# Kernel optimization log

Measured on AMD Instinct MI355X. Metric: run time of the kernel, lower is better.

## Reference

```python
import jax, jax.numpy as jnp
import numpy as np

K = 16  # kNN size (self included)
R = 4   # upsampling ratio


def _knn(pts, k):
    # pts: (B,N,3) -> idx (B,N,k); smallest distance first, so idx[:,:,0] is self
    sq = jnp.sum(pts * pts, axis=-1)
    d = sq[:, :, None] - 2.0 * jnp.einsum('bnd,bmd->bnm', pts, pts) + sq[:, None, :]
    _, idx = jax.lax.top_k(-d, k)
    return idx


def _gather(feats, idx):
    # feats (B,N,C), idx (B,N,k) -> (B,N,k,C)
    return jax.vmap(lambda f, i: f[i])(feats, idx)


def _conv1d(x, w, b):  # pointwise Conv1d: x (B,C,N)
    return jnp.einsum('oc,bcn->bon', w, x) + b[None, :, None]


def _conv2d(x, w, b):  # pointwise Conv2d: x (B,C,N,K)
    return jnp.einsum('oc,bcnk->bonk', w, x) + b[None, :, None, None]


def setup_inputs() -> dict:
    key = jax.random.key(0)
    ks = jax.random.split(key, 16)
    B, N = 2, 8192
    w = lambda k, s: jax.random.normal(k, s, jnp.float32) * 0.1
    return {
        'x': jax.random.normal(ks[0], (B, 3, N), jnp.float32),
        'mlp1_w1': w(ks[1], (32, 3)), 'mlp1_b1': jnp.zeros((32,), jnp.float32),
        'mlp1_w2': w(ks[2], (64, 32)), 'mlp1_b2': jnp.zeros((64,), jnp.float32),
        'mlp2_w1': w(ks[3], (32, 9)), 'mlp2_b1': jnp.zeros((32,), jnp.float32),
        'mlp3_w1': w(ks[4], (128, 96)), 'mlp3_b1': jnp.zeros((128,), jnp.float32),
        'mlp3_w2': w(ks[5], (12, 128)), 'mlp3_b2': jnp.zeros((12,), jnp.float32),
        'att_w1': w(ks[6], (128, 64)), 'att_b1': jnp.zeros((128,), jnp.float32),
        'att_w2': w(ks[7], (64, 128)), 'att_b2': jnp.zeros((64,), jnp.float32),
    }


def reference(x, mlp1_w1, mlp1_b1, mlp1_w2, mlp1_b2, mlp2_w1, mlp2_b1,
              mlp3_w1, mlp3_b1, mlp3_w2, mlp3_b2,
              att_w1, att_b1, att_w2, att_b2):
    B, C, N = x.shape
    pts = jnp.transpose(x, (0, 2, 1))                     # (B,N,3)
    idx = _knn(jax.lax.stop_gradient(pts), K)             # (B,N,K)

    # local 3x3 covariance features -> (B,9,N)
    nb = _gather(pts, idx)                                # (B,N,K,3)
    c = nb - jnp.mean(nb, axis=2, keepdims=True)
    cov = jnp.einsum('bnki,bnkj->bnij', c, c) / K         # (B,N,3,3)
    cov_feat = jnp.transpose(cov.reshape(B, N, 9), (0, 2, 1))

    # mlp1: 3 -> 32 -> 64, relu on both (last_act=True)
    f1 = jax.nn.relu(_conv1d(jax.nn.relu(_conv1d(x, mlp1_w1, mlp1_b1)), mlp1_w2, mlp1_b2))

    # gather neighbor features (exclude self) and form relative features
    fk = _gather(jnp.transpose(f1, (0, 2, 1)), idx[:, :, 1:])   # (B,N,K-1,64)
    f_knn = jnp.transpose(fk, (0, 3, 1, 2)) - f1[:, :, :, None]  # (B,64,N,K-1)

    # attention MLP (2D): 64 -> 128 -> 64, softmax over neighbor axis
    h = jax.nn.relu(_conv2d(f_knn, att_w1, att_b1))
    w = jax.nn.softmax(_conv2d(h, att_w2, att_b2), axis=-1)
    f_agg = jnp.sum(w * f_knn, axis=-1)                   # (B,64,N)

    # mlp2: 9 -> 32 with relu
    f_cov = jax.nn.relu(_conv1d(cov_feat, mlp2_w1, mlp2_b1))     # (B,32,N)

    f = jnp.concatenate([f_agg, f_cov], axis=1)           # (B,96,N)
    g = _conv1d(jax.nn.relu(_conv1d(f, mlp3_w1, mlp3_b1)), mlp3_w2, mlp3_b2)  # (B,3R,N)

    return jnp.tile(x, (1, 1, R)) + 0.15 * g.reshape(B, -1, R * N)
```

## Files before the change

### kernel.cpp

```cpp
#include <hip/hip_runtime.h>

#define BB 2
#define NN 8192
#define KK 16
#define QPB 64
#define PRE 256
#define CAP 16
typedef unsigned long long ull;
typedef unsigned short ushort;
#define KINF 0xFFFFFFFFFFFFFFFFULL

typedef __attribute__((ext_vector_type(8))) short short8;
typedef __attribute__((ext_vector_type(4))) float f32x4;

static __device__ __forceinline__ ushort f2bf(float f) {
    unsigned u = __float_as_uint(f);
    unsigned r = (u + 0x7FFFu + ((u >> 16) & 1u)) >> 16;
    return (ushort)r;
}
static __device__ __forceinline__ float bf2f(ushort s) {
    return __uint_as_float(((unsigned)s) << 16);
}

static __device__ __forceinline__ float distq(const float4& qp, const float4& cn) {
    return fmaf(qp.x, cn.x, fmaf(qp.y, cn.y, fmaf(qp.z, cn.z, __fadd_rn(qp.w, cn.w))));
}

__global__ __launch_bounds__(256) void prep_f1_kernel(
    const float* __restrict__ x, float4* __restrict__ pts4, float4* __restrict__ pts4n,
    const float* __restrict__ w1, const float* __restrict__ b1,
    const float* __restrict__ w2, const float* __restrict__ b2,
    ushort* __restrict__ f1)
{
    if (blockIdx.x < 64) {
        int t = blockIdx.x * 256 + threadIdx.x;
        int b = t >> 13, n = t & (NN - 1);
        float x0 = x[(b * 3 + 0) * NN + n];
        float x1 = x[(b * 3 + 1) * NN + n];
        float x2 = x[(b * 3 + 2) * NN + n];
        float sq = fmaf(x2, x2, fmaf(x1, x1, __fmul_rn(x0, x0)));
        pts4[t]  = make_float4(x0, x1, x2, sq);
        pts4n[t] = make_float4(-2.f * x0, -2.f * x1, -2.f * x2, sq);
    } else {
        int P = (blockIdx.x - 64) * 256 + threadIdx.x;
        int b = P >> 13, n = P & (NN - 1);
        float x0 = x[(b * 3 + 0) * NN + n];
        float x1 = x[(b * 3 + 1) * NN + n];
        float x2 = x[(b * 3 + 2) * NN + n];
        float h[32];
#pragma unroll
        for (int o = 0; o < 32; ++o) {
            float v = fmaf(w1[o * 3 + 2], x2, fmaf(w1[o * 3 + 1], x1, fmaf(w1[o * 3 + 0], x0, b1[o])));
            h[o] = fmaxf(v, 0.f);
        }
#pragma unroll
        for (int o4 = 0; o4 < 16; ++o4) {
            float vv[4];
#pragma unroll
            for (int u = 0; u < 4; ++u) {
                int o = o4 * 4 + u;
                float v = b2[o];
#pragma unroll
                for (int k = 0; k < 32; ++k) v = fmaf(w2[o * 32 + k], h[k], v);
                vv[u] = fmaxf(v, 0.f);
            }
            ushort4 s = { f2bf(vv[0]), f2bf(vv[1]), f2bf(vv[2]), f2bf(vv[3]) };
            *(ushort4*)(f1 + (size_t)P * 64 + o4 * 4) = s;
        }
    }
}

__global__ __launch_bounds__(512) void knn_prefix_kernel(
    const float4* __restrict__ pts4, const float4* __restrict__ pts4n,
    float* __restrict__ thrb)
{
    __shared__ float pbuf[11 * 512];
    __shared__ float smem[8 * 4 * 64];

    const int t    = threadIdx.x;
    const int wv   = t >> 6;
    const int lane = t & 63;
    const int b    = blockIdx.y;
    const int q    = blockIdx.x * QPB + lane;
    const int sl   = __builtin_amdgcn_readfirstlane(wv);

    const float4 qp = pts4[b * NN + q];
    const float4* __restrict__ cp = pts4n + (size_t)b * NN + (size_t)sl * 1024;

    float l0 = 3.0e38f, l1 = 3.0e38f, l2 = 3.0e38f, l3 = 3.0e38f;
    float curmax = 3.0e38f;
    int pend = 0;

    for (int i0 = 0; i0 < PRE; i0 += 8) {
#pragma unroll
        for (int u = 0; u < 8; ++u) {
            float d = distq(qp, cp[i0 + u]);
            pbuf[pend * 512 + t] = d;
            pend += (d < curmax) ? 1 : 0;
        }
        if (__any(pend >= 4)) {
            for (int j = 0; j < 11; ++j) {
                if (!__any(j < pend)) break;
                float v = pbuf[j * 512 + t];
                float k = (j < pend) ? v : 3.0e38f;
                bool b3 = k < l3, b2 = k < l2, b1 = k < l1, b0 = k < l0;
                l3 = b3 ? (b2 ? l2 : k) : l3;
                l2 = b2 ? (b1 ? l1 : k) : l2;
                l1 = b1 ? (b0 ? l0 : k) : l1;
                l0 = b0 ? k : l0;
            }
            pend = 0;
            curmax = l3;
        }
    }
    for (int j = 0; j < 11; ++j) {
        if (!__any(j < pend)) break;
        float v = pbuf[j * 512 + t];
        float k = (j < pend) ? v : 3.0e38f;
        bool b3 = k < l3, b2 = k < l2, b1 = k < l1, b0 = k < l0;
        l3 = b3 ? (b2 ? l2 : k) : l3;
        l2 = b2 ? (b1 ? l1 : k) : l2;
        l1 = b1 ? (b0 ? l0 : k) : l1;
        l0 = b0 ? k : l0;
    }

    __syncthreads();
    smem[(wv * 4 + 0) * 64 + lane] = l0;
    smem[(wv * 4 + 1) * 64 + lane] = l1;
    smem[(wv * 4 + 2) * 64 + lane] = l2;
    smem[(wv * 4 + 3) * 64 + lane] = l3;
    __syncthreads();

    if (t < QPB) {
        float h[8];
        int kc[8];
#pragma unroll
        for (int s = 0; s < 8; ++s) { h[s] = smem[(s * 4) * 64 + t]; kc[s] = 0; }
        float best = 3.0e38f;
        for (int o = 0; o < KK; ++o) {
            best = h[0]; int bs = 0;
#pragma unroll
            for (int s = 1; s < 8; ++s) { if (h[s] < best) { best = h[s]; bs = s; } }
#pragma unroll
            for (int s = 0; s < 8; ++s) {
                if (s == bs) {
                    kc[s]++;
                    h[s] = (kc[s] < 4) ? smem[(s * 4 + kc[s]) * 64 + t] : 3.0e38f;
                }
            }
        }
        thrb[(size_t)b * NN + blockIdx.x * QPB + t] = best;
    }
}

__global__ __launch_bounds__(512) void knn_scan_kernel(
    const float4* __restrict__ pts4, const float4* __restrict__ pts4n,
    const float* __restrict__ thrb,
    ushort* __restrict__ buf, ushort* __restrict__ cnt)
{
    const int t    = threadIdx.x;
    const int wv   = t >> 6;
    const int lane = t & 63;
    const int b    = blockIdx.y;
    const int q    = blockIdx.x * QPB + lane;
    const int s    = __builtin_amdgcn_readfirstlane(blockIdx.z * 8 + wv);

    const float4 qp = pts4[b * NN + q];
    const float thr = thrb[(size_t)b * NN + q];
    const float4* __restrict__ cp = pts4n + (size_t)b * NN + (size_t)s * 256;
    const unsigned cbase = s * 256;

    const int cell = (((int)(b * NN) + q) << 5) + s;
    ushort* __restrict__ bp = buf + (size_t)cell * CAP;
    int pend = 0;

    for (int i0 = 0; i0 < 256; i0 += 8) {
#pragma unroll
        for (int u = 0; u < 8; ++u) {
            const int ci = i0 + u;
            float d = distq(qp, cp[ci]);
            if (d <= thr) {
                bp[pend & (CAP - 1)] = (ushort)(cbase + ci);
                pend++;
            }
        }
    }
    cnt[cell] = (ushort)((pend < CAP) ? pend : CAP);
}

__global__ __launch_bounds__(256) void knn_select_kernel(
    const float4* __restrict__ pts4, const float4* __restrict__ pts4n,
    const ushort* __restrict__ buf, const ushort* __restrict__ cnt,
    int* __restrict__ iout)
{
    __shared__ ull sm3[4][8][8][KK];

    const int t = threadIdx.x;
    const int wv = t >> 6, lane = t & 63;
    const int qq = lane & 7, hh = lane >> 3;
    const int q  = (blockIdx.x * 4 + wv) * 8 + qq;
    const int b  = q >> 13;

    const float4 qp = pts4[q];
    ull list[KK];
#pragma unroll
    for (int i = 0; i < KK; ++i) list[i] = KINF;

#pragma unroll
    for (int ss = 0; ss < 4; ++ss) {
        const int s = hh * 4 + ss;
        const int cell = (q << 5) + s;
        const int n = cnt[cell];
        const ushort* bp = buf + (size_t)cell * CAP;
        for (int i = 0; i < n; ++i) {
            int id = bp[i];
            float d = distq(qp, pts4n[b * NN + id]);
            unsigned ud = __float_as_uint(d);
            ud ^= ((unsigned)((int)ud >> 31)) | 0x80000000u;
            ull k = ((ull)ud << 32) | (unsigned)id;
#pragma unroll
            for (int i2 = KK - 1; i2 > 0; --i2) {
                bool c1 = k < list[i2];
                bool c2 = k < list[i2 - 1];
                ull nd = c2 ? list[i2 - 1] : k;
                list[i2] = c1 ? nd : list[i2];
            }
            list[0] = (k < list[0]) ? k : list[0];
        }
    }

#pragma unroll
    for (int k = 0; k < KK; ++k) sm3[wv][hh][qq][k] = list[k];

    if (hh == 0) {
        ull h[8]; int kc[8];
#pragma unroll
        for (int s = 0; s < 8; ++s) { h[s] = sm3[wv][s][qq][0]; kc[s] = 0; }
        int* op = iout + (size_t)q * KK;
        for (int o = 0; o < KK; ++o) {
            ull best = h[0]; int bs = 0;
#pragma unroll
            for (int s = 1; s < 8; ++s) { if (h[s] < best) { best = h[s]; bs = s; } }
            op[o] = (int)(unsigned)(best & 0xFFFFFFFFULL);
#pragma unroll
            for (int s = 0; s < 8; ++s) {
                if (s == bs) {
                    kc[s]++;
                    h[s] = (kc[s] < KK) ? sm3[wv][s][qq][kc[s]] : KINF;
                }
            }
        }
    }
}

__global__ __launch_bounds__(256, 2) void attn_cov_kernel(
    const ushort* __restrict__ f1, const int* __restrict__ idx,
    const float* __restrict__ aw1, const float* __restrict__ ab1,
    const float* __restrict__ aw2, const float* __restrict__ ab2,
    ushort* __restrict__ fagg,
    const float4* __restrict__ pts4,
    const float* __restrict__ cw, const float* __restrict__ cb,
    ushort* __restrict__ fcov)
{
    __shared__ __align__(16) ushort w1l[128][72];
    __shared__ __align__(16) ushort w2l[64][136];
    __shared__ __align__(16) ushort fkb[4][16][72];
    __shared__ __align__(16) ushort hb[4][16][136];

    const int t = threadIdx.x;

    if (blockIdx.x >= 512) {
        int P = (blockIdx.x - 512) * 256 + t;
        int b = P >> 13;
        const int4* ip4 = (const int4*)(idx + (size_t)P * KK);
        int ids[KK];
#pragma unroll
        for (int g = 0; g < 4; ++g) {
            int4 v = ip4[g];
            ids[g * 4 + 0] = v.x; ids[g * 4 + 1] = v.y;
            ids[g * 4 + 2] = v.z; ids[g * 4 + 3] = v.w;
        }
        float px[KK], py[KK], pz[KK];
#pragma unroll
        for (int k = 0; k < KK; ++k) {
            float4 c = pts4[b * NN + ids[k]];
            px[k] = c.x; py[k] = c.y; pz[k] = c.z;
        }
        float mx = 0.f, my = 0.f, mz = 0.f;
#pragma unroll
        for (int k = 0; k < KK; ++k) { mx += px[k]; my += py[k]; mz += pz[k]; }
        mx *= (1.f / 16.f); my *= (1.f / 16.f); mz *= (1.f / 16.f);
        float c00 = 0, c01 = 0, c02 = 0, c11 = 0, c12 = 0, c22 = 0;
#pragma unroll
        for (int k = 0; k < KK; ++k) {
            float dx = px[k] - mx, dy = py[k] - my, dz = pz[k] - mz;
            c00 = fmaf(dx, dx, c00); c01 = fmaf(dx, dy, c01); c02 = fmaf(dx, dz, c02);
            c11 = fmaf(dy, dy, c11); c12 = fmaf(dy, dz, c12); c22 = fmaf(dz, dz, c22);
        }
        const float inv = 1.f / 16.f;
        float cf[9] = { c00 * inv, c01 * inv, c02 * inv,
                        c01 * inv, c11 * inv, c12 * inv,
                        c02 * inv, c12 * inv, c22 * inv };
        ushort* outp = fcov + (size_t)P * 32;
#pragma unroll
        for (int o = 0; o < 32; ++o) {
            float v = cb[o];
#pragma unroll
            for (int m = 0; m < 9; ++m) v = fmaf(cw[o * 9 + m], cf[m], v);
            outp[o] = f2bf(fmaxf(v, 0.f));
        }
        return;
    }

    const int wv = t >> 6, lane = t & 63;
    const int l15 = lane & 15, qd = lane >> 4;

    for (int i = t; i < 128 * 64; i += 256) {
        int r = i >> 6, c = i & 63;
        w1l[r][c] = f2bf(aw1[i]);
    }
    for (int i = t; i < 64 * 128; i += 256) {
        int r = i >> 7, c = i & 127;
        w2l[r][c] = f2bf(aw2[i]);
    }
    __syncthreads();

    const int W = blockIdx.x * 4 + wv;
    for (int g = 0; g < 8; ++g) {
        const int P = W * 8 + g;
        const int b = P >> 13;

        float fc = bf2f(f1[(size_t)P * 64 + lane]);
        ushort fn[15];
#pragma unroll
        for (int j = 0; j < 15; ++j) {
            int nb = idx[(size_t)P * KK + 1 + j];
            fn[j] = f1[((size_t)b * NN + nb) * 64 + lane];
        }
#pragma unroll
        for (int j = 0; j < 15; ++j) fkb[wv][j][lane] = f2bf(bf2f(fn[j]) - fc);
        fkb[wv][15][lane] = 0;

        short8 a0 = *(const short8*)&fkb[wv][l15][qd * 8];
        short8 a1 = *(const short8*)&fkb[wv][l15][32 + qd * 8];

#pragma unroll
        for (int tile = 0; tile < 8; ++tile) {
            float bv = ab1[tile * 16 + l15];
            f32x4 acc = { bv, bv, bv, bv };
            short8 b0 = *(const short8*)&w1l[tile * 16 + l15][qd * 8];
            short8 b1f = *(const short8*)&w1l[tile * 16 + l15][32 + qd * 8];
            acc = __builtin_amdgcn_mfma_f32_16x16x32_bf16(a0, b0, acc, 0, 0, 0);
            acc = __builtin_amdgcn_mfma_f32_16x16x32_bf16(a1, b1f, acc, 0, 0, 0);
#pragma unroll
            for (int reg = 0; reg < 4; ++reg)
                hb[wv][qd * 4 + reg][tile * 16 + l15] = f2bf(fmaxf(acc[reg], 0.f));
        }

        short8 a2[4];
#pragma unroll
        for (int ks = 0; ks < 4; ++ks)
            a2[ks] = *(const short8*)&hb[wv][l15][ks * 32 + qd * 8];

        f32x4 L[4];
#pragma unroll
        for (int tile = 0; tile < 4; ++tile) {
            float bv = ab2[tile * 16 + l15];
            f32x4 acc = { bv, bv, bv, bv };
#pragma unroll
            for (int ks = 0; ks < 4; ++ks) {
                short8 bf = *(const short8*)&w2l[tile * 16 + l15][ks * 32 + qd * 8];
                acc = __builtin_amdgcn_mfma_f32_16x16x32_bf16(a2[ks], bf, acc, 0, 0, 0);
            }
            L[tile] = acc;
        }

        float fa[4];
#pragma unroll
        for (int tile = 0; tile < 4; ++tile) {
            float m1 = -3.0e38f;
#pragma unroll
            for (int reg = 0; reg < 4; ++reg)
                if (qd * 4 + reg < 15) m1 = fmaxf(m1, L[tile][reg]);
            m1 = fmaxf(m1, __shfl_xor(m1, 16));
            m1 = fmaxf(m1, __shfl_xor(m1, 32));
            float e[4], ssum = 0.f;
#pragma unroll
            for (int reg = 0; reg < 4; ++reg) {
                bool valid = (qd * 4 + reg < 15);
                e[reg] = valid ? __expf(L[tile][reg] - m1) : 0.f;
                ssum += e[reg];
            }
            ssum += __shfl_xor(ssum, 16);
            ssum += __shfl_xor(ssum, 32);
            float part = 0.f;
#pragma unroll
            for (int reg = 0; reg < 4; ++reg) {
                float fkv = bf2f(fkb[wv][qd * 4 + reg][tile * 16 + l15]);
                part = fmaf(e[reg], fkv, part);
            }
            part += __shfl_xor(part, 16);
            part += __shfl_xor(part, 32);
            fa[tile] = part / ssum;
        }
        if (qd == 0) {
#pragma unroll
            for (int tile = 0; tile < 4; ++tile)
                fagg[(size_t)P * 64 + tile * 16 + l15] = f2bf(fa[tile]);
        }
    }
}

__global__ __launch_bounds__(256) void mlp3_kernel(
    const ushort* __restrict__ fagg, const ushort* __restrict__ fcov,
    const float* __restrict__ w1, const float* __restrict__ b1,
    const float* __restrict__ w2, const float* __restrict__ b2,
    const float* __restrict__ x, float* __restrict__ out)
{
    __shared__ __align__(16) ushort fb[4][16][104];
    __shared__ __align__(16) ushort hb[4][16][136];

    const int t = threadIdx.x;
    const int wv = t >> 6, lane = t & 63;
    const int l15 = lane & 15, qd = lane >> 4;

    short8 w1f[8][3];
#pragma unroll
    for (int tile = 0; tile < 8; ++tile)
#pragma unroll
        for (int ks = 0; ks < 3; ++ks) {
            const float* p = w1 + ((size_t)(tile * 16 + l15) * 96 + ks * 32 + qd * 8);
            float4 A = *(const float4*)p, B = *(const float4*)(p + 4);
            short8 f;
            f[0] = f2bf(A.x); f[1] = f2bf(A.y); f[2] = f2bf(A.z); f[3] = f2bf(A.w);
            f[4] = f2bf(B.x); f[5] = f2bf(B.y); f[6] = f2bf(B.z); f[7] = f2bf(B.w);
            w1f[tile][ks] = f;
        }
    short8 w2f[4];
#pragma unroll
    for (int ks = 0; ks < 4; ++ks) {
        short8 f = {};
        if (l15 < 12) {
            const float* p = w2 + ((size_t)l15 * 128 + ks * 32 + qd * 8);
            float4 A = *(const float4*)p, B = *(const float4*)(p + 4);
            f[0] = f2bf(A.x); f[1] = f2bf(A.y); f[2] = f2bf(A.z); f[3] = f2bf(A.w);
            f[4] = f2bf(B.x); f[5] = f2bf(B.y); f[6] = f2bf(B.z); f[7] = f2bf(B.w);
        }
        w2f[ks] = f;
    }

    const int T = blockIdx.x * 4 + wv;

    {
        const int pt = lane >> 2, c4 = lane & 3;
        const ushort* fap = fagg + ((size_t)(T * 16 + pt) * 64 + c4 * 16);
        *(short8*)&fb[wv][pt][c4 * 16]     = *(const short8*)(fap);
        *(short8*)&fb[wv][pt][c4 * 16 + 8] = *(const short8*)(fap + 8);
        const ushort* fcp = fcov + ((size_t)(T * 16 + pt) * 32 + c4 * 8);
        *(short8*)&fb[wv][pt][64 + c4 * 8] = *(const short8*)(fcp);
    }

    short8 a[3];
#pragma unroll
    for (int ks = 0; ks < 3; ++ks)
        a[ks] = *(const short8*)&fb[wv][l15][ks * 32 + qd * 8];

#pragma unroll
    for (int tile = 0; tile < 8; ++tile) {
        float bv = b1[tile * 16 + l15];
        f32x4 acc = { bv, bv, bv, bv };
#pragma unroll
        for (int ks = 0; ks < 3; ++ks)
            acc = __builtin_amdgcn_mfma_f32_16x16x32_bf16(a[ks], w1f[tile][ks], acc, 0, 0, 0);
#pragma unroll
        for (int reg = 0; reg < 4; ++reg)
            hb[wv][qd * 4 + reg][tile * 16 + l15] = f2bf(fmaxf(acc[reg], 0.f));
    }

    short8 a2[4];
#pragma unroll
    for (int ks = 0; ks < 4; ++ks)
        a2[ks] = *(const short8*)&hb[wv][l15][ks * 32 + qd * 8];

    float bv2 = (l15 < 12) ? b2[l15] : 0.f;
    f32x4 acc = { bv2, bv2, bv2, bv2 };
#pragma unroll
    for (int ks = 0; ks < 4; ++ks)
        acc = __builtin_amdgcn_mfma_f32_16x16x32_bf16(a2[ks], w2f[ks], acc, 0, 0, 0);

    if (l15 < 12) {
        const int c = l15 >> 2, rr = l15 & 3;
#pragma unroll
        for (int reg = 0; reg < 4; ++reg) {
            int P = T * 16 + qd * 4 + reg;
            int b = P >> 13, n = P & (NN - 1);
            float xv = x[((size_t)b * 3 + c) * NN + n];
            out[(((size_t)b * 3 + c) * 4 + rr) * NN + n] = xv + 0.15f * acc[reg];
        }
    }
}

extern "C" void kernel_launch(void* const* d_in, const int* in_sizes, int n_in,
                              void* d_out, int out_size, void* d_ws, size_t ws_size,
                              hipStream_t stream)
{
    (void)in_sizes; (void)n_in; (void)out_size; (void)ws_size;
    const float* x    = (const float*)d_in[0];
    const float* m1w1 = (const float*)d_in[1];
    const float* m1b1 = (const float*)d_in[2];
    const float* m1w2 = (const float*)d_in[3];
    const float* m1b2 = (const float*)d_in[4];
    const float* m2w1 = (const float*)d_in[5];
    const float* m2b1 = (const float*)d_in[6];
    const float* m3w1 = (const float*)d_in[7];
    const float* m3b1 = (const float*)d_in[8];
    const float* m3w2 = (const float*)d_in[9];
    const float* m3b2 = (const float*)d_in[10];
    const float* aw1  = (const float*)d_in[11];
    const float* ab1  = (const float*)d_in[12];
    const float* aw2  = (const float*)d_in[13];
    const float* ab2  = (const float*)d_in[14];
    float* out = (float*)d_out;

    char* ws = (char*)d_ws;
    float4* pts4  = (float4*)(ws + 0);
    float4* pts4n = (float4*)(ws + 262144);
    float*  thrb  = (float*)(ws + 524288);
    int*    idxb  = (int*)  (ws + 589824);
    ushort* cntb  = (ushort*)(ws + 1638400);
    ushort* bufb  = (ushort*)(ws + 2686976);
    ushort* f1b   = (ushort*)(ws + 19464192);
    ushort* fagg  = (ushort*)(ws + 21561344);
    ushort* fcov  = (ushort*)(ws + 23658496);

    prep_f1_kernel<<<128, 256, 0, stream>>>(x, pts4, pts4n, m1w1, m1b1, m1w2, m1b2, f1b);
    knn_prefix_kernel<<<dim3(NN / QPB, BB), 512, 0, stream>>>(pts4, pts4n, thrb);
    knn_scan_kernel<<<dim3(NN / QPB, BB, 4), 512, 0, stream>>>(pts4, pts4n, thrb, bufb, cntb);
    knn_select_kernel<<<512, 256, 0, stream>>>(pts4, pts4n, bufb, cntb, idxb);
    attn_cov_kernel<<<576, 256, 0, stream>>>(f1b, idxb, aw1, ab1, aw2, ab2, fagg,
                                             pts4, m2w1, m2b1, fcov);
    mlp3_kernel<<<256, 256, 0, stream>>>(fagg, fcov, m3w1, m3b1, m3w2, m3b2, x, out);
}
```

Measured before the change: 262.8 us.

## Fuse kNN select with attention/cov kernel and ballot-compact the scan

```diff
diff --git a/kernel.cpp b/kernel.cpp
--- a/kernel.cpp
+++ b/kernel.cpp
@@ -162,124 +162,124 @@
     const int wv   = t >> 6;
     const int lane = t & 63;
     const int b    = blockIdx.y;
-    const int q    = blockIdx.x * QPB + lane;
     const int s    = __builtin_amdgcn_readfirstlane(blockIdx.z * 8 + wv);
-
-    const float4 qp = pts4[b * NN + q];
-    const float thr = thrb[(size_t)b * NN + q];
-    const float4* __restrict__ cp = pts4n + (size_t)b * NN + (size_t)s * 256;
+    const int q0   = blockIdx.x * QPB;
     const unsigned cbase = s * 256;
-
-    const int cell = (((int)(b * NN) + q) << 5) + s;
-    ushort* __restrict__ bp = buf + (size_t)cell * CAP;
-    int pend = 0;
-
-    for (int i0 = 0; i0 < 256; i0 += 8) {
-#pragma unroll
-        for (int u = 0; u < 8; ++u) {
-            const int ci = i0 + u;
-            float d = distq(qp, cp[ci]);
-            if (d <= thr) {
-                bp[pend & (CAP - 1)] = (ushort)(cbase + ci);
-                pend++;
-            }
-        }
-    }
-    cnt[cell] = (ushort)((pend < CAP) ? pend : CAP);
-}
-
-__global__ __launch_bounds__(256) void knn_select_kernel(
+    const ull lmask = (lane == 0) ? 0ull : (~0ull >> (64 - lane));
+
+    const float4* __restrict__ cp = pts4n + (size_t)b * NN + cbase;
+    float4 c0 = cp[lane], c1 = cp[64 + lane], c2 = cp[128 + lane], c3 = cp[192 + lane];
+
+    const float4* __restrict__ qpb = pts4 + (size_t)b * NN + q0;
+    const float*  __restrict__ thp = thrb + (size_t)b * NN + q0;
+
+    for (int qi = 0; qi < QPB; ++qi) {
+        const float4 qp = qpb[qi];
+        const float thr = thp[qi];
+        const int cell = (((b * NN) + q0 + qi) << 5) + s;
+        ushort* __restrict__ bp = buf + (size_t)cell * CAP;
+        int pend = 0;
+#pragma unroll
+        for (int k = 0; k < 4; ++k) {
+            float4 c = (k == 0) ? c0 : (k == 1) ? c1 : (k == 2) ? c2 : c3;
+            float d = distq(qp, c);
+            bool pass = (d <= thr);
+            ull m = __ballot(pass);
+            int slot = pend + (int)__popcll(m & lmask);
+            if (pass && slot < CAP) bp[slot] = (ushort)(cbase + k * 64 + lane);
+            pend += (int)__popcll(m);
+        }
+        if (lane == 0) cnt[cell] = (ushort)((pend < CAP) ? pend : CAP);
+    }
+}
+
+__global__ __launch_bounds__(256, 2) void sel_attn_cov_kernel(
     const float4* __restrict__ pts4, const float4* __restrict__ pts4n,
     const ushort* __restrict__ buf, const ushort* __restrict__ cnt,
-    int* __restrict__ iout)
+    const ushort* __restrict__ f1,
+    const float* __restrict__ aw1, const float* __restrict__ ab1,
+    const float* __restrict__ aw2, const float* __restrict__ ab2,
+    const float* __restrict__ cw, const float* __restrict__ cb,
+    ushort* __restrict__ fagg, ushort* __restrict__ fcov)
 {
-    __shared__ ull sm3[4][8][8][KK];
+    __shared__ __align__(16) ull sm3[4][8][8][KK];
+    __shared__ __align__(16) ushort w2l[64][136];
+    __shared__ int idxl[32][KK];
+
+    ushort (*fkb)[16][72]  = (ushort(*)[16][72])sm3;
+    ushort (*hb)[16][136]  = (ushort(*)[16][136])((char*)sm3 + 9216);
 
     const int t = threadIdx.x;
     const int wv = t >> 6, lane = t & 63;
-    const int qq = lane & 7, hh = lane >> 3;
-    const int q  = (blockIdx.x * 4 + wv) * 8 + qq;
-    const int b  = q >> 13;
-
-    const float4 qp = pts4[q];
-    ull list[KK];
-#pragma unroll
-    for (int i = 0; i < KK; ++i) list[i] = KINF;
-
-#pragma unroll
-    for (int ss = 0; ss < 4; ++ss) {
-        const int s = hh * 4 + ss;
-        const int cell = (q << 5) + s;
-        const int n = cnt[cell];
-        const ushort* bp = buf + (size_t)cell * CAP;
-        for (int i = 0; i < n; ++i) {
-            int id = bp[i];
-            float d = distq(qp, pts4n[b * NN + id]);
-            unsigned ud = __float_as_uint(d);
-            ud ^= ((unsigned)((int)ud >> 31)) | 0x80000000u;
-            ull k = ((ull)ud << 32) | (unsigned)id;
-#pragma unroll
-            for (int i2 = KK - 1; i2 > 0; --i2) {
-                bool c1 = k < list[i2];
-                bool c2 = k < list[i2 - 1];
-                ull nd = c2 ? list[i2 - 1] : k;
-                list[i2] = c1 ? nd : list[i2];
-            }
-            list[0] = (k < list[0]) ? k : list[0];
-        }
-    }
-
-#pragma unroll
-    for (int k = 0; k < KK; ++k) sm3[wv][hh][qq][k] = list[k];
-
-    if (hh == 0) {
-        ull h[8]; int kc[8];
-#pragma unroll
-        for (int s = 0; s < 8; ++s) { h[s] = sm3[wv][s][qq][0]; kc[s] = 0; }
-        int* op = iout + (size_t)q * KK;
-        for (int o = 0; o < KK; ++o) {
-            ull best = h[0]; int bs = 0;
-#pragma unroll
-            for (int s = 1; s < 8; ++s) { if (h[s] < best) { best = h[s]; bs = s; } }
-            op[o] = (int)(unsigned)(best & 0xFFFFFFFFULL);
-#pragma unroll
-            for (int s = 0; s < 8; ++s) {
-                if (s == bs) {
-                    kc[s]++;
-                    h[s] = (kc[s] < KK) ? sm3[wv][s][qq][kc[s]] : KINF;
+
+    for (int i = t; i < 64 * 128; i += 256) {
+        int r = i >> 7, c = i & 127;
+        w2l[r][c] = f2bf(aw2[i]);
+    }
+
+    {
+        const int qq = lane & 7, hh = lane >> 3;
+        const int q  = blockIdx.x * 32 + wv * 8 + qq;
+        const int b  = q >> 13;
+
+        const float4 qp = pts4[q];
+        ull list[KK];
+#pragma unroll
+        for (int i = 0; i < KK; ++i) list[i] = KINF;
+
+#pragma unroll
+        for (int ss = 0; ss < 4; ++ss) {
+            const int s = hh * 4 + ss;
+            const int cell = (q << 5) + s;
+            const int n = cnt[cell];
+            const ushort* bp = buf + (size_t)cell * CAP;
+            for (int i = 0; i < n; ++i) {
+                int id = bp[i];
+                float d = distq(qp, pts4n[b * NN + id]);
+                unsigned ud = __float_as_uint(d);
+                ud ^= ((unsigned)((int)ud >> 31)) | 0x80000000u;
+                ull k = ((ull)ud << 32) | (unsigned)id;
+#pragma unroll
+                for (int i2 = KK - 1; i2 > 0; --i2) {
+                    bool c1 = k < list[i2];
+                    bool c2 = k < list[i2 - 1];
+                    ull nd = c2 ? list[i2 - 1] : k;
+                    list[i2] = c1 ? nd : list[i2];
                 }
-            }
-        }
-    }
-}
-
-__global__ __launch_bounds__(256, 2) void attn_cov_kernel(
-    const ushort* __restrict__ f1, const int* __restrict__ idx,
-    const float* __restrict__ aw1, const float* __restrict__ ab1,
-    const float* __restrict__ aw2, const float* __restrict__ ab2,
-    ushort* __restrict__ fagg,
-    const float4* __restrict__ pts4,
-    const float* __restrict__ cw, const float* __restrict__ cb,
-    ushort* __restrict__ fcov)
-{
-    __shared__ __align__(16) ushort w1l[128][72];
-    __shared__ __align__(16) ushort w2l[64][136];
-    __shared__ __align__(16) ushort fkb[4][16][72];
-    __shared__ __align__(16) ushort hb[4][16][136];
-
-    const int t = threadIdx.x;
-
-    if (blockIdx.x >= 512) {
-        int P = (blockIdx.x - 512) * 256 + t;
+                list[0] = (k < list[0]) ? k : list[0];
+            }
+        }
+
+#pragma unroll
+        for (int k = 0; k < KK; ++k) sm3[wv][hh][qq][k] = list[k];
+
+        if (hh == 0) {
+            ull h[8]; int kc[8];
+#pragma unroll
+            for (int s = 0; s < 8; ++s) { h[s] = sm3[wv][s][qq][0]; kc[s] = 0; }
+            for (int o = 0; o < KK; ++o) {
+                ull best = h[0]; int bs = 0;
+#pragma unroll
+                for (int s = 1; s < 8; ++s) { if (h[s] < best) { best = h[s]; bs = s; } }
+                idxl[wv * 8 + qq][o] = (int)(unsigned)(best & 0xFFFFFFFFULL);
+#pragma unroll
+                for (int s = 0; s < 8; ++s) {
+                    if (s == bs) {
+                        kc[s]++;
+                        h[s] = (kc[s] < KK) ? sm3[wv][s][qq][kc[s]] : KINF;
+                    }
+                }
+            }
+        }
+    }
+    __syncthreads();
+
+    if (t < 32) {
+        int P = blockIdx.x * 32 + t;
         int b = P >> 13;
-        const int4* ip4 = (const int4*)(idx + (size_t)P * KK);
         int ids[KK];
 #pragma unroll
-        for (int g = 0; g < 4; ++g) {
-            int4 v = ip4[g];
-            ids[g * 4 + 0] = v.x; ids[g * 4 + 1] = v.y;
-            ids[g * 4 + 2] = v.z; ids[g * 4 + 3] = v.w;
-        }
+        for (int k = 0; k < KK; ++k) ids[k] = idxl[t][k];
         float px[KK], py[KK], pz[KK];
 #pragma unroll
         for (int k = 0; k < KK; ++k) {
@@ -309,32 +309,32 @@
             for (int m = 0; m < 9; ++m) v = fmaf(cw[o * 9 + m], cf[m], v);
             outp[o] = f2bf(fmaxf(v, 0.f));
         }
-        return;
-    }
-
-    const int wv = t >> 6, lane = t & 63;
+    }
+
     const int l15 = lane & 15, qd = lane >> 4;
 
-    for (int i = t; i < 128 * 64; i += 256) {
-        int r = i >> 6, c = i & 63;
-        w1l[r][c] = f2bf(aw1[i]);
-    }
-    for (int i = t; i < 64 * 128; i += 256) {
-        int r = i >> 7, c = i & 127;
-        w2l[r][c] = f2bf(aw2[i]);
-    }
-    __syncthreads();
-
-    const int W = blockIdx.x * 4 + wv;
+    short8 w1f[8][2];
+#pragma unroll
+    for (int tile = 0; tile < 8; ++tile)
+#pragma unroll
+        for (int ks = 0; ks < 2; ++ks) {
+            const float4* p = (const float4*)(aw1 + ((tile * 16 + l15) * 64 + ks * 32 + qd * 8));
+            float4 A = p[0], B = p[1];
+            short8 f;
+            f[0] = f2bf(A.x); f[1] = f2bf(A.y); f[2] = f2bf(A.z); f[3] = f2bf(A.w);
+            f[4] = f2bf(B.x); f[5] = f2bf(B.y); f[6] = f2bf(B.z); f[7] = f2bf(B.w);
+            w1f[tile][ks] = f;
+        }
+
     for (int g = 0; g < 8; ++g) {
-        const int P = W * 8 + g;
+        const int P = blockIdx.x * 32 + wv * 8 + g;
         const int b = P >> 13;
 
         float fc = bf2f(f1[(size_t)P * 64 + lane]);
         ushort fn[15];
 #pragma unroll
         for (int j = 0; j < 15; ++j) {
-            int nb = idx[(size_t)P * KK + 1 + j];
+            int nb = idxl[wv * 8 + g][1 + j];
             fn[j] = f1[((size_t)b * NN + nb) * 64 + lane];
         }
 #pragma unroll
@@ -348,10 +348,8 @@
         for (int tile = 0; tile < 8; ++tile) {
             float bv = ab1[tile * 16 + l15];
             f32x4 acc = { bv, bv, bv, bv };
-            short8 b0 = *(const short8*)&w1l[tile * 16 + l15][qd * 8];
-            short8 b1f = *(const short8*)&w1l[tile * 16 + l15][32 + qd * 8];
-            acc = __builtin_amdgcn_mfma_f32_16x16x32_bf16(a0, b0, acc, 0, 0, 0);
-            acc = __builtin_amdgcn_mfma_f32_16x16x32_bf16(a1, b1f, acc, 0, 0, 0);
+            acc = __builtin_amdgcn_mfma_f32_16x16x32_bf16(a0, w1f[tile][0], acc, 0, 0, 0);
+            acc = __builtin_amdgcn_mfma_f32_16x16x32_bf16(a1, w1f[tile][1], acc, 0, 0, 0);
 #pragma unroll
             for (int reg = 0; reg < 4; ++reg)
                 hb[wv][qd * 4 + reg][tile * 16 + l15] = f2bf(fmaxf(acc[reg], 0.f));
@@ -526,18 +524,17 @@
     float4* pts4  = (float4*)(ws + 0);
     float4* pts4n = (float4*)(ws + 262144);
     float*  thrb  = (float*)(ws + 524288);
-    int*    idxb  = (int*)  (ws + 589824);
-    ushort* cntb  = (ushort*)(ws + 1638400);
-    ushort* bufb  = (ushort*)(ws + 2686976);
-    ushort* f1b   = (ushort*)(ws + 19464192);
-    ushort* fagg  = (ushort*)(ws + 21561344);
-    ushort* fcov  = (ushort*)(ws + 23658496);
+    ushort* cntb  = (ushort*)(ws + 589824);
+    ushort* bufb  = (ushort*)(ws + 1638400);
+    ushort* f1b   = (ushort*)(ws + 18415616);
+    ushort* fagg  = (ushort*)(ws + 20512768);
+    ushort* fcov  = (ushort*)(ws + 22609920);
 
     prep_f1_kernel<<<128, 256, 0, stream>>>(x, pts4, pts4n, m1w1, m1b1, m1w2, m1b2, f1b);
     knn_prefix_kernel<<<dim3(NN / QPB, BB), 512, 0, stream>>>(pts4, pts4n, thrb);
     knn_scan_kernel<<<dim3(NN / QPB, BB, 4), 512, 0, stream>>>(pts4, pts4n, thrb, bufb, cntb);
-    knn_select_kernel<<<512, 256, 0, stream>>>(pts4, pts4n, bufb, cntb, idxb);
-    attn_cov_kernel<<<576, 256, 0, stream>>>(f1b, idxb, aw1, ab1, aw2, ab2, fagg,
-                                             pts4, m2w1, m2b1, fcov);
+    sel_attn_cov_kernel<<<512, 256, 0, stream>>>(pts4, pts4n, bufb, cntb, f1b,
+                                                 aw1, ab1, aw2, ab2, m2w1, m2b1,
+                                                 fagg, fcov);
     mlp3_kernel<<<256, 256, 0, stream>>>(fagg, fcov, m3w1, m3b1, m3w2, m3b2, x, out);
 }
```

Measured after the change: 268.5 us. 1.02x slower.

## Fuse kNN prefix-threshold and scan kernels with ballot-compacted candidate writes

Applied to the files above, without the earlier changes.

```diff
diff --git a/kernel.cpp b/kernel.cpp
--- a/kernel.cpp
+++ b/kernel.cpp
@@ -70,122 +70,120 @@
     }
 }
 
-__global__ __launch_bounds__(512) void knn_prefix_kernel(
+__global__ __launch_bounds__(512) void knn_ps_kernel(
     const float4* __restrict__ pts4, const float4* __restrict__ pts4n,
-    float* __restrict__ thrb)
+    ushort* __restrict__ buf, ushort* __restrict__ cnt)
 {
     __shared__ float pbuf[11 * 512];
     __shared__ float smem[8 * 4 * 64];
+    __shared__ float thrl[QPB];
 
     const int t    = threadIdx.x;
     const int wv   = t >> 6;
     const int lane = t & 63;
     const int b    = blockIdx.y;
-    const int q    = blockIdx.x * QPB + lane;
+    const int q0   = blockIdx.x * QPB;
     const int sl   = __builtin_amdgcn_readfirstlane(wv);
 
-    const float4 qp = pts4[b * NN + q];
-    const float4* __restrict__ cp = pts4n + (size_t)b * NN + (size_t)sl * 1024;
-
-    float l0 = 3.0e38f, l1 = 3.0e38f, l2 = 3.0e38f, l3 = 3.0e38f;
-    float curmax = 3.0e38f;
-    int pend = 0;
-
-    for (int i0 = 0; i0 < PRE; i0 += 8) {
-#pragma unroll
-        for (int u = 0; u < 8; ++u) {
-            float d = distq(qp, cp[i0 + u]);
-            pbuf[pend * 512 + t] = d;
-            pend += (d < curmax) ? 1 : 0;
-        }
-        if (__any(pend >= 4)) {
-            for (int j = 0; j < 11; ++j) {
-                if (!__any(j < pend)) break;
-                float v = pbuf[j * 512 + t];
-                float k = (j < pend) ? v : 3.0e38f;
-                bool b3 = k < l3, b2 = k < l2, b1 = k < l1, b0 = k < l0;
-                l3 = b3 ? (b2 ? l2 : k) : l3;
-                l2 = b2 ? (b1 ? l1 : k) : l2;
-                l1 = b1 ? (b0 ? l0 : k) : l1;
-                l0 = b0 ? k : l0;
-            }
-            pend = 0;
-            curmax = l3;
-        }
-    }
-    for (int j = 0; j < 11; ++j) {
-        if (!__any(j < pend)) break;
-        float v = pbuf[j * 512 + t];
-        float k = (j < pend) ? v : 3.0e38f;
-        bool b3 = k < l3, b2 = k < l2, b1 = k < l1, b0 = k < l0;
-        l3 = b3 ? (b2 ? l2 : k) : l3;
-        l2 = b2 ? (b1 ? l1 : k) : l2;
-        l1 = b1 ? (b0 ? l0 : k) : l1;
-        l0 = b0 ? k : l0;
-    }
-
-    __syncthreads();
-    smem[(wv * 4 + 0) * 64 + lane] = l0;
-    smem[(wv * 4 + 1) * 64 + lane] = l1;
-    smem[(wv * 4 + 2) * 64 + lane] = l2;
-    smem[(wv * 4 + 3) * 64 + lane] = l3;
-    __syncthreads();
-
-    if (t < QPB) {
-        float h[8];
-        int kc[8];
-#pragma unroll
-        for (int s = 0; s < 8; ++s) { h[s] = smem[(s * 4) * 64 + t]; kc[s] = 0; }
-        float best = 3.0e38f;
-        for (int o = 0; o < KK; ++o) {
-            best = h[0]; int bs = 0;
-#pragma unroll
-            for (int s = 1; s < 8; ++s) { if (h[s] < best) { best = h[s]; bs = s; } }
-#pragma unroll
-            for (int s = 0; s < 8; ++s) {
-                if (s == bs) {
-                    kc[s]++;
-                    h[s] = (kc[s] < 4) ? smem[(s * 4 + kc[s]) * 64 + t] : 3.0e38f;
+    {
+        const float4 qp = pts4[b * NN + q0 + lane];
+        const float4* __restrict__ cp = pts4n + (size_t)b * NN + (size_t)sl * 1024;
+
+        float l0 = 3.0e38f, l1 = 3.0e38f, l2 = 3.0e38f, l3 = 3.0e38f;
+        float curmax = 3.0e38f;
+        int pend = 0;
+
+        for (int i0 = 0; i0 < PRE; i0 += 8) {
+#pragma unroll
+            for (int u = 0; u < 8; ++u) {
+                float d = distq(qp, cp[i0 + u]);
+                pbuf[pend * 512 + t] = d;
+                pend += (d < curmax) ? 1 : 0;
+            }
+            if (__any(pend >= 4)) {
+                for (int j = 0; j < 11; ++j) {
+                    if (!__any(j < pend)) break;
+                    float v = pbuf[j * 512 + t];
+                    float k = (j < pend) ? v : 3.0e38f;
+                    bool b3 = k < l3, b2 = k < l2, b1 = k < l1, b0 = k < l0;
+                    l3 = b3 ? (b2 ? l2 : k) : l3;
+                    l2 = b2 ? (b1 ? l1 : k) : l2;
+                    l1 = b1 ? (b0 ? l0 : k) : l1;
+                    l0 = b0 ? k : l0;
                 }
-            }
-        }
-        thrb[(size_t)b * NN + blockIdx.x * QPB + t] = best;
-    }
-}
-
-__global__ __launch_bounds__(512) void knn_scan_kernel(
-    const float4* __restrict__ pts4, const float4* __restrict__ pts4n,
-    const float* __restrict__ thrb,
-    ushort* __restrict__ buf, ushort* __restrict__ cnt)
-{
-    const int t    = threadIdx.x;
-    const int wv   = t >> 6;
-    const int lane = t & 63;
-    const int b    = blockIdx.y;
-    const int q    = blockIdx.x * QPB + lane;
-    const int s    = __builtin_amdgcn_readfirstlane(blockIdx.z * 8 + wv);
-
-    const float4 qp = pts4[b * NN + q];
-    const float thr = thrb[(size_t)b * NN + q];
-    const float4* __restrict__ cp = pts4n + (size_t)b * NN + (size_t)s * 256;
-    const unsigned cbase = s * 256;
-
-    const int cell = (((int)(b * NN) + q) << 5) + s;
-    ushort* __restrict__ bp = buf + (size_t)cell * CAP;
-    int pend = 0;
-
-    for (int i0 = 0; i0 < 256; i0 += 8) {
-#pragma unroll
-        for (int u = 0; u < 8; ++u) {
-            const int ci = i0 + u;
-            float d = distq(qp, cp[ci]);
-            if (d <= thr) {
-                bp[pend & (CAP - 1)] = (ushort)(cbase + ci);
-                pend++;
-            }
-        }
-    }
-    cnt[cell] = (ushort)((pend < CAP) ? pend : CAP);
+                pend = 0;
+                curmax = l3;
+            }
+        }
+        for (int j = 0; j < 11; ++j) {
+            if (!__any(j < pend)) break;
+            float v = pbuf[j * 512 + t];
+            float k = (j < pend) ? v : 3.0e38f;
+            bool b3 = k < l3, b2 = k < l2, b1 = k < l1, b0 = k < l0;
+            l3 = b3 ? (b2 ? l2 : k) : l3;
+            l2 = b2 ? (b1 ? l1 : k) : l2;
+            l1 = b1 ? (b0 ? l0 : k) : l1;
+            l0 = b0 ? k : l0;
+        }
+
+        __syncthreads();
+        smem[(wv * 4 + 0) * 64 + lane] = l0;
+        smem[(wv * 4 + 1) * 64 + lane] = l1;
+        smem[(wv * 4 + 2) * 64 + lane] = l2;
+        smem[(wv * 4 + 3) * 64 + lane] = l3;
+        __syncthreads();
+
+        if (t < QPB) {
+            float h[8];
+            int kc[8];
+#pragma unroll
+            for (int s = 0; s < 8; ++s) { h[s] = smem[(s * 4) * 64 + t]; kc[s] = 0; }
+            float best = 3.0e38f;
+            for (int o = 0; o < KK; ++o) {
+                best = h[0]; int bs = 0;
+#pragma unroll
+                for (int s = 1; s < 8; ++s) { if (h[s] < best) { best = h[s]; bs = s; } }
+#pragma unroll
+                for (int s = 0; s < 8; ++s) {
+                    if (s == bs) {
+                        kc[s]++;
+                        h[s] = (kc[s] < 4) ? smem[(s * 4 + kc[s]) * 64 + t] : 3.0e38f;
+                    }
+                }
+            }
+            thrl[t] = best;
+        }
+        __syncthreads();
+    }
+
+    const ull lmask = (lane == 0) ? 0ull : (~0ull >> (64 - lane));
+    const float4* __restrict__ qpb = pts4 + (size_t)b * NN + q0;
+
+    for (int z = 0; z < 4; ++z) {
+        const int s = __builtin_amdgcn_readfirstlane(z * 8 + wv);
+        const unsigned cbase = s * 256;
+        const float4* __restrict__ cp = pts4n + (size_t)b * NN + cbase;
+        float4 c0 = cp[lane], c1 = cp[64 + lane], c2 = cp[128 + lane], c3 = cp[192 + lane];
+
+        for (int qi = 0; qi < QPB; ++qi) {
+            const float4 qp = qpb[qi];
+            const float thr = thrl[qi];
+            const int cell = (((b * NN) + q0 + qi) << 5) + s;
+            ushort* __restrict__ bp = buf + (size_t)cell * CAP;
+            int pend = 0;
+#pragma unroll
+            for (int k = 0; k < 4; ++k) {
+                float4 c = (k == 0) ? c0 : (k == 1) ? c1 : (k == 2) ? c2 : c3;
+                float d = distq(qp, c);
+                bool pass = (d <= thr);
+                ull m = __ballot(pass);
+                int slot = pend + (int)__popcll(m & lmask);
+                if (pass && slot < CAP) bp[slot] = (ushort)(cbase + k * 64 + lane);
+                pend += (int)__popcll(m);
+            }
+            if (lane == 0) cnt[cell] = (ushort)((pend < CAP) ? pend : CAP);
+        }
+    }
 }
 
 __global__ __launch_bounds__(256) void knn_select_kernel(
@@ -193,7 +191,7 @@
     const ushort* __restrict__ buf, const ushort* __restrict__ cnt,
     int* __restrict__ iout)
 {
-    __shared__ ull sm3[4][8][8][KK];
+    __shared__ ull sm3[4][8][8][KK + 1];
 
     const int t = threadIdx.x;
     const int wv = t >> 6, lane = t & 63;
@@ -525,17 +523,15 @@
     char* ws = (char*)d_ws;
     float4* pts4  = (float4*)(ws + 0);
     float4* pts4n = (float4*)(ws + 262144);
-    float*  thrb  = (float*)(ws + 524288);
-    int*    idxb  = (int*)  (ws + 589824);
-    ushort* cntb  = (ushort*)(ws + 1638400);
-    ushort* bufb  = (ushort*)(ws + 2686976);
-    ushort* f1b   = (ushort*)(ws + 19464192);
-    ushort* fagg  = (ushort*)(ws + 21561344);
-    ushort* fcov  = (ushort*)(ws + 23658496);
+    int*    idxb  = (int*)  (ws + 524288);
+    ushort* cntb  = (ushort*)(ws + 1572864);
+    ushort* bufb  = (ushort*)(ws + 2621440);
+    ushort* f1b   = (ushort*)(ws + 19398656);
+    ushort* fagg  = (ushort*)(ws + 21495808);
+    ushort* fcov  = (ushort*)(ws + 23592960);
 
     prep_f1_kernel<<<128, 256, 0, stream>>>(x, pts4, pts4n, m1w1, m1b1, m1w2, m1b2, f1b);
-    knn_prefix_kernel<<<dim3(NN / QPB, BB), 512, 0, stream>>>(pts4, pts4n, thrb);
-    knn_scan_kernel<<<dim3(NN / QPB, BB, 4), 512, 0, stream>>>(pts4, pts4n, thrb, bufb, cntb);
+    knn_ps_kernel<<<dim3(NN / QPB, BB), 512, 0, stream>>>(pts4, pts4n, bufb, cntb);
     knn_select_kernel<<<512, 256, 0, stream>>>(pts4, pts4n, bufb, cntb, idxb);
     attn_cov_kernel<<<576, 256, 0, stream>>>(f1b, idxb, aw1, ab1, aw2, ab2, fagg,
                                              pts4, m2w1, m2b1, fcov);
```

New measurement: 304.9 us. 1.16x slower.
